# Performance work log

Measured on AMD Instinct MI355X. Metric: run time of the kernel, lower is better.

## Reference

```python
import jax, jax.numpy as jnp
import numpy as np

N_NODES = 50000
N_EDGES = 800000
N_GRAPHS = 512
NEG_SLOPE = 0.2  # PyG GATv2Conv default negative_slope

# layer dims: (in_feat, out_channels, heads)
LAYER_DIMS = [(11, 64, 3), (192, 64, 3), (192, 64, 3), (192, 20, 1)]


def setup_inputs() -> dict:
    key = jax.random.key(0)
    ks = jax.random.split(key, 4 + 6 * len(LAYER_DIMS))
    inp = {}
    inp["x"] = jax.random.normal(ks[0], (N_NODES, 11), jnp.float32)
    src = jax.random.randint(ks[1], (N_EDGES,), 0, N_NODES, dtype=jnp.int32)
    dst = jax.random.randint(ks[2], (N_EDGES,), 0, N_NODES, dtype=jnp.int32)
    inp["edge_index"] = jnp.stack([src, dst])
    inp["batch"] = jnp.sort(jax.random.randint(ks[3], (N_NODES,), 0, N_GRAPHS, dtype=jnp.int32))
    ki = 4
    for li, (fi, ch, h) in enumerate(LAYER_DIMS):
        fo = h * ch
        s = 1.0 / np.sqrt(fi)
        inp[f"Wl{li}"] = jax.random.normal(ks[ki + 0], (fo, fi), jnp.float32) * s
        inp[f"bl{li}"] = jnp.zeros((fo,), jnp.float32)
        inp[f"Wr{li}"] = jax.random.normal(ks[ki + 1], (fo, fi), jnp.float32) * s
        inp[f"br{li}"] = jnp.zeros((fo,), jnp.float32)
        inp[f"att{li}"] = jax.random.normal(ks[ki + 2], (h, ch), jnp.float32) * (1.0 / np.sqrt(ch))
        inp[f"b{li}"] = jnp.zeros((fo,), jnp.float32)
        ki += 6
    return inp


def gatv2_layer(x, src, dst, Wl, bl, Wr, br, att, bias, heads, ch):
    """PyG GATv2Conv (concat=True): e = att . leaky_relu(lin_l(x_j)+lin_r(x_i)),
    alpha = softmax over incoming edges of each dst node, out = sum alpha * lin_l(x_j)."""
    N = x.shape[0]
    xl = (x @ Wl.T + bl).reshape(N, heads, ch)  # source transform [N,H,C]
    xr = (x @ Wr.T + br).reshape(N, heads, ch)  # target transform [N,H,C]
    m = xl[src] + xr[dst]                        # [E,H,C] edge-wise gather
    e = jnp.einsum("ehc,hc->eh", jax.nn.leaky_relu(m, NEG_SLOPE), att)  # [E,H]
    emax = jax.ops.segment_max(e, dst, num_segments=N)   # per-dst softmax (stable)
    p = jnp.exp(e - emax[dst])
    denom = jax.ops.segment_sum(p, dst, num_segments=N)
    alpha = p / denom[dst]                        # [E,H]
    out = jax.ops.segment_sum(xl[src] * alpha[..., None], dst, num_segments=N)
    return out.reshape(N, heads * ch) + bias


def reference(x, edge_index, batch,
              Wl0, bl0, Wr0, br0, att0, b0,
              Wl1, bl1, Wr1, br1, att1, b1,
              Wl2, bl2, Wr2, br2, att2, b2,
              Wl3, bl3, Wr3, br3, att3, b3):
    N = x.shape[0]
    loop = jnp.arange(N, dtype=edge_index.dtype)  # add_self_loops=True
    src = jnp.concatenate([edge_index[0], loop])
    dst = jnp.concatenate([edge_index[1], loop])
    h = gatv2_layer(x, src, dst, Wl0, bl0, Wr0, br0, att0, b0, 3, 64)
    h = jax.nn.relu(h)
    h = gatv2_layer(h, src, dst, Wl1, bl1, Wr1, br1, att1, b1, 3, 64)
    h = jax.nn.relu(h)
    h = gatv2_layer(h, src, dst, Wl2, bl2, Wr2, br2, att2, b2, 3, 64)
    h = jax.nn.relu(h)
    h = gatv2_layer(h, src, dst, Wl3, bl3, Wr3, br3, att3, b3, 1, 20)
    # global_add_pool
    return jax.ops.segment_sum(h, batch, num_segments=N_GRAPHS)  # [G, 20]
```

## Files before the change

### kernel.cpp

```cpp
#include <hip/hip_runtime.h>

#define NN 50000
#define NE 800000
#define NT 850000
#define NG 512
#define NSB 49

typedef __attribute__((ext_vector_type(8))) short bf16x8;
typedef __attribute__((ext_vector_type(4))) float f32x4;


template <int CTRL>
__device__ __forceinline__ float dpp_add(float x) {
  int y = __builtin_amdgcn_update_dpp(0, __float_as_int(x), CTRL, 0xF, 0xF, true);
  return x + __int_as_float(y);
}
template <int CTRL>
__device__ __forceinline__ float dpp_max(float x) {
  int y = __builtin_amdgcn_update_dpp(0, __float_as_int(x), CTRL, 0xF, 0xF, true);
  return fmaxf(x, __int_as_float(y));
}

__device__ __forceinline__ float swz16(float x) {
  return __int_as_float(__builtin_amdgcn_ds_swizzle(__float_as_int(x), 0x401F));
}

__device__ __forceinline__ float rowsum16(float x) {
  x = dpp_add<0xB1>(x);
  x = dpp_add<0x4E>(x);
  x = dpp_add<0x124>(x);
  x = dpp_add<0x128>(x);
  return x;
}
__device__ __forceinline__ float quadsum4(float x) {
  x = dpp_add<0xB1>(x);
  x = dpp_add<0x4E>(x);
  return x;
}
__device__ __forceinline__ float xg_sum(float x) {
  x += swz16(x);
  auto p = __builtin_amdgcn_permlane32_swap(__float_as_uint(x), __float_as_uint(x), false, false);
  return __uint_as_float(p[0]) + __uint_as_float(p[1]);
}
__device__ __forceinline__ float xg_max(float x) {
  x = fmaxf(x, swz16(x));
  auto p = __builtin_amdgcn_permlane32_swap(__float_as_uint(x), __float_as_uint(x), false, false);
  return fmaxf(__uint_as_float(p[0]), __uint_as_float(p[1]));
}
__device__ __forceinline__ float xq_sum(float x) {
  x = dpp_add<0x124>(x);
  x = dpp_add<0x128>(x);
  return xg_sum(x);
}
__device__ __forceinline__ float xq_max(float x) {
  x = dpp_max<0x124>(x);
  x = dpp_max<0x128>(x);
  return xg_max(x);
}

__device__ __forceinline__ float exp2_fast(float x) {
#if __has_builtin(__builtin_amdgcn_exp2f)
  return __builtin_amdgcn_exp2f(x);
#else
  return exp2f(x);
#endif
}

__device__ __forceinline__ float lrelu(float t) { return fmaxf(t, 0.2f * t); }

__device__ __forceinline__ unsigned int f2bf(float f) {
  unsigned int u = __float_as_uint(f);
  u = (u + 0x7FFFu + ((u >> 16) & 1u)) >> 16;
  return u;
}
__device__ __forceinline__ float bf_lo(unsigned int u) { return __uint_as_float(u << 16); }
__device__ __forceinline__ float bf_hi(unsigned int u) { return __uint_as_float(u & 0xFFFF0000u); }
__device__ __forceinline__ float4 bf2f4(uint2 u) {
  return make_float4(bf_lo(u.x), bf_hi(u.x), bf_lo(u.y), bf_hi(u.y));
}

__device__ __forceinline__ void pk_l(float2& d, float2 a, float2 b) {
  asm("v_pk_fma_f32 %0, %1, %2, %0 op_sel_hi:[0,1,1]" : "+v"(d) : "v"(a), "v"(b));
}
__device__ __forceinline__ void pk_h(float2& d, float2 a, float2 b) {
  asm("v_pk_fma_f32 %0, %1, %2, %0 op_sel:[1,0,0]" : "+v"(d) : "v"(a), "v"(b));
}


__global__ void k_hist(const int* __restrict__ dst, int* __restrict__ cnt) {
  int i = blockIdx.x * blockDim.x + threadIdx.x;
  if (i < NT) {
    int d = (i < NE) ? dst[i] : (i - NE);
    atomicAdd(&cnt[d], 1);
  }
}

__global__ __launch_bounds__(1024)
void k_scanA(const int* __restrict__ cnt, int* __restrict__ offs, int* __restrict__ bsum) {
  __shared__ int sh[1024];
  int tid = threadIdx.x;
  int idx = blockIdx.x * 1024 + tid;
  int v = (idx < NN) ? cnt[idx] : 0;
  sh[tid] = v;
  __syncthreads();
  for (int off = 1; off < 1024; off <<= 1) {
    int t = (tid >= off) ? sh[tid - off] : 0;
    __syncthreads();
    sh[tid] += t;
    __syncthreads();
  }
  if (idx < NN) offs[idx] = sh[tid] - v;
  if (tid == 1023) bsum[blockIdx.x] = sh[1023];
}

__global__ void k_scanB(int* __restrict__ bsum, int* __restrict__ offs) {
  int tot = 0;
#pragma unroll 7
  for (int i = 0; i < NSB; ++i) {
    int v = bsum[i];
    bsum[i] = tot;
    tot += v;
  }
  offs[NN] = tot;
}

__global__ __launch_bounds__(1024)
void k_scanC(int* __restrict__ offs, const int* __restrict__ bsum) {
  int idx = blockIdx.x * 1024 + threadIdx.x;
  if (idx < NN) offs[idx] += bsum[blockIdx.x];
}

__global__ void k_scatter(const int* __restrict__ src, const int* __restrict__ dst,
                          const int* __restrict__ offs, int* __restrict__ cur,
                          int* __restrict__ srt) {
  int i = blockIdx.x * blockDim.x + threadIdx.x;
  if (i < NT) {
    int s, d;
    if (i < NE) { s = src[i]; d = dst[i]; }
    else        { s = d = i - NE; }
    int pos = offs[d] + atomicAdd(&cur[d], 1);
    srt[pos] = s;
  }
}

__global__ void k_goffs(const int* __restrict__ batch, int* __restrict__ goffs) {
  int i = blockIdx.x * 256 + threadIdx.x;
  if (i >= NN) return;
  int b = batch[i];
  if (i == 0) {
    for (int g = 0; g <= b; ++g) goffs[g] = 0;
  } else {
    int pb = batch[i - 1];
    for (int g = pb + 1; g <= b; ++g) goffs[g] = i;
  }
  if (i == NN - 1) {
    for (int g = b + 1; g <= NG; ++g) goffs[g] = NN;
  }
}


__global__ void k_cvtW(const float* __restrict__ a, const float* __restrict__ b,
                       const float* __restrict__ c, const float* __restrict__ d,
                       const float* __restrict__ e, const float* __restrict__ f,
                       unsigned short* __restrict__ out) {
  int i = blockIdx.x * 256 + threadIdx.x;
  if (i >= 155136) return;
  float v;
  if      (i < 36864)  v = a[i];
  else if (i < 73728)  v = b[i - 36864];
  else if (i < 110592) v = c[i - 73728];
  else if (i < 147456) v = d[i - 110592];
  else if (i < 151296) v = e[i - 147456];
  else                 v = f[i - 151296];
  out[i] = (unsigned short)f2bf(v);
}


#define LSTR 200

__global__ __launch_bounds__(256)
void k_gemm_mfma2(const unsigned short* __restrict__ Abf,
                  const unsigned short* __restrict__ W1bf,
                  const unsigned short* __restrict__ W2bf,
                  const float* __restrict__ bias1, const float* __restrict__ bias2,
                  unsigned short* __restrict__ C1, unsigned short* __restrict__ C2,
                  int M, int FO) {
  __shared__ unsigned short Al[64 * LSTR];
  __shared__ unsigned short Bl[2][64 * LSTR];
  int tid = threadIdx.x;
  int mb = blockIdx.x * 64;
  int nb = blockIdx.y * 64;

  {
    int r = tid >> 2, q = tid & 3;
    int ga = min(mb + r, M - 1);
    int gb = min(nb + r, FO - 1);
    const unsigned short* pA = Abf  + (size_t)ga * 192 + q * 48;
    const unsigned short* p1 = W1bf + (size_t)gb * 192 + q * 48;
    const unsigned short* p2 = W2bf + (size_t)gb * 192 + q * 48;
    unsigned short* lA = Al + r * LSTR + q * 48;
    unsigned short* l1 = Bl[0] + r * LSTR + q * 48;
    unsigned short* l2 = Bl[1] + r * LSTR + q * 48;
#pragma unroll
    for (int i = 0; i < 6; ++i) {
      *(bf16x8*)(lA + i * 8) = *(const bf16x8*)(pA + i * 8);
      *(bf16x8*)(l1 + i * 8) = *(const bf16x8*)(p1 + i * 8);
      *(bf16x8*)(l2 + i * 8) = *(const bf16x8*)(p2 + i * 8);
    }
  }
  __syncthreads();

  int l = tid & 63, wid = tid >> 6;
  int wr = (wid >> 1) * 32, wc = (wid & 1) * 32;
  int lr = l & 15, lk = (l >> 4) * 8;

  f32x4 acc[2][2][2];
#pragma unroll
  for (int a = 0; a < 2; ++a)
#pragma unroll
    for (int b = 0; b < 2; ++b)
#pragma unroll
      for (int c = 0; c < 2; ++c) acc[a][b][c] = (f32x4){0.f, 0.f, 0.f, 0.f};

  const unsigned short* pa0 = Al + (wr + 0 + lr) * LSTR + lk;
  const unsigned short* pa1 = Al + (wr + 16 + lr) * LSTR + lk;
  const unsigned short* p10 = Bl[0] + (wc + 0 + lr) * LSTR + lk;
  const unsigned short* p11 = Bl[0] + (wc + 16 + lr) * LSTR + lk;
  const unsigned short* p20 = Bl[1] + (wc + 0 + lr) * LSTR + lk;
  const unsigned short* p21 = Bl[1] + (wc + 16 + lr) * LSTR + lk;
#pragma unroll
  for (int kt = 0; kt < 6; ++kt) {
    bf16x8 a0 = *(const bf16x8*)(pa0 + kt * 32);
    bf16x8 a1 = *(const bf16x8*)(pa1 + kt * 32);
    bf16x8 b10 = *(const bf16x8*)(p10 + kt * 32);
    bf16x8 b11 = *(const bf16x8*)(p11 + kt * 32);
    bf16x8 b20 = *(const bf16x8*)(p20 + kt * 32);
    bf16x8 b21 = *(const bf16x8*)(p21 + kt * 32);
    acc[0][0][0] = __builtin_amdgcn_mfma_f32_16x16x32_bf16(a0, b10, acc[0][0][0], 0, 0, 0);
    acc[0][0][1] = __builtin_amdgcn_mfma_f32_16x16x32_bf16(a0, b11, acc[0][0][1], 0, 0, 0);
    acc[0][1][0] = __builtin_amdgcn_mfma_f32_16x16x32_bf16(a1, b10, acc[0][1][0], 0, 0, 0);
    acc[0][1][1] = __builtin_amdgcn_mfma_f32_16x16x32_bf16(a1, b11, acc[0][1][1], 0, 0, 0);
    acc[1][0][0] = __builtin_amdgcn_mfma_f32_16x16x32_bf16(a0, b20, acc[1][0][0], 0, 0, 0);
    acc[1][0][1] = __builtin_amdgcn_mfma_f32_16x16x32_bf16(a0, b21, acc[1][0][1], 0, 0, 0);
    acc[1][1][0] = __builtin_amdgcn_mfma_f32_16x16x32_bf16(a1, b20, acc[1][1][0], 0, 0, 0);
    acc[1][1][1] = __builtin_amdgcn_mfma_f32_16x16x32_bf16(a1, b21, acc[1][1][1], 0, 0, 0);
  }

  int rb = (l >> 4) * 4;
#pragma unroll
  for (int mt = 0; mt < 2; ++mt) {
    unsigned short* C = mt == 0 ? C1 : C2;
    const float* bias = mt == 0 ? bias1 : bias2;
#pragma unroll
    for (int fn = 0; fn < 2; ++fn) {
      int col = nb + wc + fn * 16 + lr;
      if (col >= FO) continue;
      float bv = bias[col];
#pragma unroll
      for (int fm = 0; fm < 2; ++fm) {
        const f32x4& av = acc[mt][fm][fn];
#pragma unroll
        for (int i = 0; i < 4; ++i) {
          int row = mb + wr + fm * 16 + rb + i;
          if (row < M) C[(size_t)row * FO + col] = (unsigned short)f2bf(av[i] + bv);
        }
      }
    }
  }
}


__global__ __launch_bounds__(256)
void k_gemm_dual(const float* __restrict__ A, int M, int K, int FO,
                 const float* __restrict__ W1, const float* __restrict__ bias1,
                 const float* __restrict__ W2, const float* __restrict__ bias2,
                 unsigned short* __restrict__ C1, unsigned short* __restrict__ C2) {
  constexpr int CT = 16;
  constexpr int BN = CT * 4;
  constexpr int BR = (256 / CT) * 8;
  constexpr int AF4 = BR / 64;
  __shared__ float As[16][BR + 4];
  __shared__ float Bs[2][16][BN + 4];

  int tid = threadIdx.x;
  int tx = tid % CT, ty = tid / CT;
  int mb = blockIdx.x * BR, nb = blockIdx.y * BN;
  int nkt = (K + 15) >> 4;

  float4 sa[AF4], sb1, sb2;

  auto ldrow = [&](const float* P, int row, int lim, int k0, int kq) -> float4 {
    float4 v = make_float4(0.f, 0.f, 0.f, 0.f);
    if (row < lim) {
      float t[4];
#pragma unroll
      for (int i = 0; i < 4; ++i)
        t[i] = (k0 + kq + i < K) ? P[(size_t)row * K + k0 + kq + i] : 0.f;
      v = make_float4(t[0], t[1], t[2], t[3]);
    }
    return v;
  };

  auto loadg = [&](int kt) {
    int k0 = kt * 16;
#pragma unroll
    for (int q = 0; q < AF4; ++q) {
      int f4 = q * 256 + tid;
      sa[q] = ldrow(A, mb + (f4 >> 2), M, k0, (f4 & 3) * 4);
    }
    int row = tid >> 2, kq = (tid & 3) * 4;
    sb1 = ldrow(W1, nb + row, FO, k0, kq);
    sb2 = ldrow(W2, nb + row, FO, k0, kq);
  };

  auto stlds = [&]() {
#pragma unroll
    for (int q = 0; q < AF4; ++q) {
      int f4 = q * 256 + tid;
      int row = f4 >> 2, kq = (f4 & 3) * 4;
      As[kq + 0][row] = sa[q].x; As[kq + 1][row] = sa[q].y;
      As[kq + 2][row] = sa[q].z; As[kq + 3][row] = sa[q].w;
    }
    int row = tid >> 2, kq = (tid & 3) * 4;
    Bs[0][kq + 0][row] = sb1.x; Bs[0][kq + 1][row] = sb1.y;
    Bs[0][kq + 2][row] = sb1.z; Bs[0][kq + 3][row] = sb1.w;
    Bs[1][kq + 0][row] = sb2.x; Bs[1][kq + 1][row] = sb2.y;
    Bs[1][kq + 2][row] = sb2.z; Bs[1][kq + 3][row] = sb2.w;
  };

  float2 c1[8][2], c2[8][2];
#pragma unroll
  for (int r = 0; r < 8; ++r)
#pragma unroll
    for (int j = 0; j < 2; ++j) {
      c1[r][j] = make_float2(0.f, 0.f);
      c2[r][j] = make_float2(0.f, 0.f);
    }

  loadg(0);
  stlds();
  __syncthreads();

  for (int t = 0;;) {
#pragma unroll
    for (int k = 0; k < 16; ++k) {
      float4 av0 = *(const float4*)&As[k][ty * 8 + 0];
      float4 av1 = *(const float4*)&As[k][ty * 8 + 4];
      float4 bv1 = *(const float4*)&Bs[0][k][tx * 4];
      float4 bv2 = *(const float4*)&Bs[1][k][tx * 4];
      float2 f1a = make_float2(bv1.x, bv1.y), f1b = make_float2(bv1.z, bv1.w);
      float2 f2a = make_float2(bv2.x, bv2.y), f2b = make_float2(bv2.z, bv2.w);
      float2 a01 = make_float2(av0.x, av0.y), a23 = make_float2(av0.z, av0.w);
      float2 a45 = make_float2(av1.x, av1.y), a67 = make_float2(av1.z, av1.w);
#define PKROW(rp, a)                                                       \
      pk_l(c1[2 * rp + 0][0], a, f1a); pk_l(c1[2 * rp + 0][1], a, f1b);    \
      pk_h(c1[2 * rp + 1][0], a, f1a); pk_h(c1[2 * rp + 1][1], a, f1b);    \
      pk_l(c2[2 * rp + 0][0], a, f2a); pk_l(c2[2 * rp + 0][1], a, f2b);    \
      pk_h(c2[2 * rp + 1][0], a, f2a); pk_h(c2[2 * rp + 1][1], a, f2b);
      PKROW(0, a01) PKROW(1, a23) PKROW(2, a45) PKROW(3, a67)
#undef PKROW
    }
    if (++t == nkt) break;
    loadg(t);
    __syncthreads();
    stlds();
    __syncthreads();
  }

  int col = nb + tx * 4;
  if (col < FO) {
    float4 bb1 = *(const float4*)&bias1[col];
    float4 bb2 = *(const float4*)&bias2[col];
#pragma unroll
    for (int r = 0; r < 8; ++r) {
      int m = mb + ty * 8 + r;
      if (m >= M) continue;
      uint2 o1, o2;
      o1.x = f2bf(c1[r][0].x + bb1.x) | (f2bf(c1[r][0].y + bb1.y) << 16);
      o1.y = f2bf(c1[r][1].x + bb1.z) | (f2bf(c1[r][1].y + bb1.w) << 16);
      o2.x = f2bf(c2[r][0].x + bb2.x) | (f2bf(c2[r][0].y + bb2.y) << 16);
      o2.y = f2bf(c2[r][1].x + bb2.z) | (f2bf(c2[r][1].y + bb2.w) << 16);
      *(uint2*)&C1[(size_t)m * FO + col] = o1;
      *(uint2*)&C2[(size_t)m * FO + col] = o2;
    }
  }
}


__global__ __launch_bounds__(256)
void k_gat3(const unsigned short* __restrict__ xl, const unsigned short* __restrict__ xr,
            const float* __restrict__ att, const float* __restrict__ bias,
            const int* __restrict__ offs, const int* __restrict__ srt,
            unsigned short* __restrict__ obf, int relu) {
  const float L2E = 1.4426950408889634f;
  int lane = threadIdx.x & 63;
  int grp = lane >> 4, lg = lane & 15;
  int n = blockIdx.x * 4 + (threadIdx.x >> 6);
  if (n >= NN) return;

  float4 xrv[3], atv[3];
#pragma unroll
  for (int h = 0; h < 3; ++h) {
    xrv[h] = bf2f4(*(const uint2*)(xr + (size_t)n * 192 + h * 64 + lg * 4));
    float4 a = *(const float4*)&att[h * 64 + lg * 4];
    atv[h] = make_float4(a.x * L2E, a.y * L2E, a.z * L2E, a.w * L2E);
  }
  float m[3] = {-1e30f, -1e30f, -1e30f}, d[3] = {0.f, 0.f, 0.f};
  float4 acc[3];
#pragma unroll
  for (int h = 0; h < 3; ++h) acc[h] = make_float4(0.f, 0.f, 0.f, 0.f);

  int e0 = offs[n], e1 = offs[n + 1];
  int nch = (e1 - e0 + 3) >> 2;

  uint2 Rc[3];
  bool vc;
  int j = e0 + grp;
  {
    int jj = min(j, e1 - 1);
    int s = srt[jj];
    const unsigned short* b = xl + (size_t)s * 192 + lg * 4;
    Rc[0] = *(const uint2*)(b);
    Rc[1] = *(const uint2*)(b + 64);
    Rc[2] = *(const uint2*)(b + 128);
    vc = j < e1;
  }
  for (int it = 0; it < nch; ++it) {
    uint2 Rn[3];
    bool vn = false;
    int jn = j + 4;
    if (it + 1 < nch) {
      int jj = min(jn, e1 - 1);
      int s = srt[jj];
      const unsigned short* b = xl + (size_t)s * 192 + lg * 4;
      Rn[0] = *(const uint2*)(b);
      Rn[1] = *(const uint2*)(b + 64);
      Rn[2] = *(const uint2*)(b + 128);
      vn = jn < e1;
    }
    float4 Xc[3];
    Xc[0] = bf2f4(Rc[0]); Xc[1] = bf2f4(Rc[1]); Xc[2] = bf2f4(Rc[2]);
    float part[3];
#pragma unroll
    for (int h = 0; h < 3; ++h) {
      float t = lrelu(Xc[h].x + xrv[h].x);
      float pa = t * atv[h].x;
      t = lrelu(Xc[h].y + xrv[h].y); pa = fmaf(t, atv[h].y, pa);
      t = lrelu(Xc[h].z + xrv[h].z); pa = fmaf(t, atv[h].z, pa);
      t = lrelu(Xc[h].w + xrv[h].w); pa = fmaf(t, atv[h].w, pa);
      part[h] = pa;
    }
#pragma unroll
    for (int h = 0; h < 3; ++h) {
      part[h] = rowsum16(part[h]);
      part[h] = vc ? part[h] : -1e30f;
    }
    float g = fmaxf(fmaxf(part[0] - m[0], part[1] - m[1]), part[2] - m[2]);
    if (__any(g > 11.0f)) {
#pragma unroll
      for (int h = 0; h < 3; ++h) {
        float nm = fmaxf(m[h], part[h]);
        float sc = exp2_fast(m[h] - nm);
        d[h] *= sc;
        acc[h].x *= sc; acc[h].y *= sc; acc[h].z *= sc; acc[h].w *= sc;
        m[h] = nm;
      }
    }
#pragma unroll
    for (int h = 0; h < 3; ++h) {
      float p = vc ? exp2_fast(part[h] - m[h]) : 0.f;
      d[h] += p;
      acc[h].x = fmaf(p, Xc[h].x, acc[h].x);
      acc[h].y = fmaf(p, Xc[h].y, acc[h].y);
      acc[h].z = fmaf(p, Xc[h].z, acc[h].z);
      acc[h].w = fmaf(p, Xc[h].w, acc[h].w);
    }
    Rc[0] = Rn[0]; Rc[1] = Rn[1]; Rc[2] = Rn[2];
    vc = vn; j = jn;
  }

#pragma unroll
  for (int h = 0; h < 3; ++h) {
    float nm = xg_max(m[h]);
    float sc = exp2_fast(m[h] - nm);
    float D = xg_sum(d[h] * sc);
    float A0 = xg_sum(acc[h].x * sc);
    float A1 = xg_sum(acc[h].y * sc);
    float A2 = xg_sum(acc[h].z * sc);
    float A3 = xg_sum(acc[h].w * sc);
    if (grp == 0) {
      float4 bb = *(const float4*)&bias[h * 64 + lg * 4];
      float inv = 1.0f / D;
      float v0 = fmaf(A0, inv, bb.x);
      float v1 = fmaf(A1, inv, bb.y);
      float v2 = fmaf(A2, inv, bb.z);
      float v3 = fmaf(A3, inv, bb.w);
      if (relu) {
        v0 = fmaxf(v0, 0.f); v1 = fmaxf(v1, 0.f);
        v2 = fmaxf(v2, 0.f); v3 = fmaxf(v3, 0.f);
      }
      unsigned int lo = f2bf(v0) | (f2bf(v1) << 16);
      unsigned int hi = f2bf(v2) | (f2bf(v3) << 16);
      *(uint2*)(obf + (size_t)n * 192 + h * 64 + lg * 4) = make_uint2(lo, hi);
    }
  }
}


__global__ __launch_bounds__(256)
void k_gat1(const unsigned short* __restrict__ xl, const unsigned short* __restrict__ xr,
            const float* __restrict__ att, const float* __restrict__ bias,
            const int* __restrict__ offs, const int* __restrict__ srt,
            float* __restrict__ hout) {
  const float L2E = 1.4426950408889634f;
  int lane = threadIdx.x & 63;
  int grp = lane >> 2, lg = lane & 3;
  int n = blockIdx.x * 4 + (threadIdx.x >> 6);
  if (n >= NN) return;

  float xrv[5], atv[5];
#pragma unroll
  for (int i = 0; i < 5; ++i) {
    xrv[i] = bf_lo(xr[(size_t)n * 20 + lg * 5 + i]);
    atv[i] = att[lg * 5 + i] * L2E;
  }
  float m = -1e30f, d = 0.f, a[5] = {0.f, 0.f, 0.f, 0.f, 0.f};

  int e0 = offs[n], e1 = offs[n + 1];
  int nch = (e1 - e0 + 15) >> 4;

  float Xc[5];
  bool vc;
  int j = e0 + grp;
  {
    int jj = min(j, e1 - 1);
    int s = srt[jj];
    const unsigned short* b = xl + (size_t)s * 20 + lg * 5;
#pragma unroll
    for (int i = 0; i < 5; ++i) Xc[i] = bf_lo(b[i]);
    vc = j < e1;
  }
  for (int it = 0; it < nch; ++it) {
    float Xn[5] = {0.f, 0.f, 0.f, 0.f, 0.f};
    bool vn = false;
    int jn = j + 16;
    if (it + 1 < nch) {
      int jj = min(jn, e1 - 1);
      int s = srt[jj];
      const unsigned short* b = xl + (size_t)s * 20 + lg * 5;
#pragma unroll
      for (int i = 0; i < 5; ++i) Xn[i] = bf_lo(b[i]);
      vn = jn < e1;
    }
    float pa = lrelu(Xc[0] + xrv[0]) * atv[0];
#pragma unroll
    for (int i = 1; i < 5; ++i) pa = fmaf(lrelu(Xc[i] + xrv[i]), atv[i], pa);
    pa = quadsum4(pa);
    pa = vc ? pa : -1e30f;
    if (__any(pa - m > 11.0f)) {
      float nm = fmaxf(m, pa);
      float sc = exp2_fast(m - nm);
      d *= sc;
#pragma unroll
      for (int i = 0; i < 5; ++i) a[i] *= sc;
      m = nm;
    }
    float p = vc ? exp2_fast(pa - m) : 0.f;
    d += p;
#pragma unroll
    for (int i = 0; i < 5; ++i) a[i] = fmaf(p, Xc[i], a[i]);
#pragma unroll
    for (int i = 0; i < 5; ++i) Xc[i] = Xn[i];
    vc = vn; j = jn;
  }

  float nm = xq_max(m);
  float sc = exp2_fast(m - nm);
  float D = xq_sum(d * sc);
  float A[5];
#pragma unroll
  for (int i = 0; i < 5; ++i) A[i] = xq_sum(a[i] * sc);
  if (grp == 0) {
    float inv = 1.0f / D;
    float* o = hout + (size_t)n * 20 + lg * 5;
#pragma unroll
    for (int i = 0; i < 5; ++i)
      o[i] = fmaf(A[i], inv, bias[lg * 5 + i]);
  }
}


__global__ __launch_bounds__(64)
void k_pool(const float* __restrict__ h, const int* __restrict__ goffs,
            float* __restrict__ out) {
  int g = blockIdx.x;
  int lane = threadIdx.x;
  if (lane >= 20) return;
  int s = goffs[g], e = goffs[g + 1];
  float sum = 0.f;
  for (int r = s; r < e; ++r) sum += h[(size_t)r * 20 + lane];
  out[g * 20 + lane] = sum;
}


extern "C" void kernel_launch(void* const* d_in, const int* in_sizes, int n_in,
                              void* d_out, int out_size, void* d_ws, size_t ws_size,
                              hipStream_t stream) {
  const float* x = (const float*)d_in[0];
  const int* src = (const int*)d_in[1];
  const int* dst = src + NE;
  const int* batch = (const int*)d_in[2];
  const float *Wl[4], *bl[4], *Wr[4], *br[4], *att[4], *bb[4];
  for (int li = 0; li < 4; ++li) {
    Wl[li]  = (const float*)d_in[3 + li * 6 + 0];
    bl[li]  = (const float*)d_in[3 + li * 6 + 1];
    Wr[li]  = (const float*)d_in[3 + li * 6 + 2];
    br[li]  = (const float*)d_in[3 + li * 6 + 3];
    att[li] = (const float*)d_in[3 + li * 6 + 4];
    bb[li]  = (const float*)d_in[3 + li * 6 + 5];
  }

  char* p = (char*)d_ws;
  auto alloc = [&](size_t bytes) {
    char* r = p;
    p += (bytes + 255) & ~(size_t)255;
    return r;
  };
  unsigned short* xlbf = (unsigned short*)alloc((size_t)NN * 192 * 2);
  unsigned short* xrbf = (unsigned short*)alloc((size_t)NN * 192 * 2);
  unsigned short* hbf  = (unsigned short*)alloc((size_t)NN * 192 * 2);
  unsigned short* wb   = (unsigned short*)alloc((size_t)155136 * 2);
  int* srt   = (int*)alloc((size_t)NT * 4);
  int* offs  = (int*)alloc((size_t)(NN + 1) * 4);
  int* cnt   = (int*)alloc((size_t)NN * 4);
  int* cur   = (int*)alloc((size_t)NN * 4);
  int* bsum  = (int*)alloc((size_t)NSB * 4);
  int* goffs = (int*)alloc((size_t)(NG + 1) * 4);
  float* hpool = (float*)alloc((size_t)NN * 20 * 4);

  hipMemsetAsync(cnt, 0, (size_t)NN * 4, stream);
  hipMemsetAsync(cur, 0, (size_t)NN * 4, stream);

  k_hist<<<(NT + 255) / 256, 256, 0, stream>>>(dst, cnt);
  k_scanA<<<NSB, 1024, 0, stream>>>(cnt, offs, bsum);
  k_scanB<<<1, 1, 0, stream>>>(bsum, offs);
  k_scanC<<<NSB, 1024, 0, stream>>>(offs, bsum);
  k_scatter<<<(NT + 255) / 256, 256, 0, stream>>>(src, dst, offs, cur, srt);
  k_goffs<<<(NN + 255) / 256, 256, 0, stream>>>(batch, goffs);
  k_cvtW<<<(155136 + 255) / 256, 256, 0, stream>>>(Wl[1], Wr[1], Wl[2], Wr[2], Wl[3], Wr[3], wb);

  {
    dim3 g((NN + 127) / 128, 3);
    k_gemm_dual<<<g, 256, 0, stream>>>(x, NN, 11, 192, Wl[0], bl[0], Wr[0], br[0], xlbf, xrbf);
    k_gat3<<<(NN + 3) / 4, 256, 0, stream>>>(xlbf, xrbf, att[0], bb[0], offs, srt, hbf, 1);
  }
  {
    dim3 gm((NN + 63) / 64, 3);
    k_gemm_mfma2<<<gm, 256, 0, stream>>>(hbf, wb + 0, wb + 36864, bl[1], br[1], xlbf, xrbf, NN, 192);
    k_gat3<<<(NN + 3) / 4, 256, 0, stream>>>(xlbf, xrbf, att[1], bb[1], offs, srt, hbf, 1);
    k_gemm_mfma2<<<gm, 256, 0, stream>>>(hbf, wb + 73728, wb + 110592, bl[2], br[2], xlbf, xrbf, NN, 192);
    k_gat3<<<(NN + 3) / 4, 256, 0, stream>>>(xlbf, xrbf, att[2], bb[2], offs, srt, hbf, 1);
  }
  {
    dim3 gm((NN + 63) / 64, 1);
    k_gemm_mfma2<<<gm, 256, 0, stream>>>(hbf, wb + 147456, wb + 151296, bl[3], br[3], xlbf, xrbf, NN, 20);
    k_gat1<<<(NN + 3) / 4, 256, 0, stream>>>(xlbf, xrbf, att[3], bb[3], offs, srt, hpool);
    k_pool<<<NG, 64, 0, stream>>>(hpool, goffs, (float*)d_out);
  }
}
```

Measured before the change: 523.4 us.

## Drop LDS staging in GEMM, pack GAT math, deepen gather prefetch

The MFMA GEMM kernel now feeds its MFMA operands straight from global memory instead of staging A and both weight tiles in shared memory behind a barrier. The GATv2 aggregation kernel rewrites its per-edge math with packed v_pk_fma_f32 operations on float2 pairs. It also switches from a one-deep to a two-deep software prefetch of neighbour rows, alternating two register buffers. The aims are to remove LDS traffic and the sync, halve VALU instruction count, and hide more gather latency, at the cost of redundant global loads across waves and higher register pressure.

Measured after the change: 583.4 us. +11.5%, slower.

```diff
diff --git a/kernel.cpp b/kernel.cpp
--- a/kernel.cpp
+++ b/kernel.cpp
@@ -75,8 +75,11 @@
 }
 __device__ __forceinline__ float bf_lo(unsigned int u) { return __uint_as_float(u << 16); }
 __device__ __forceinline__ float bf_hi(unsigned int u) { return __uint_as_float(u & 0xFFFF0000u); }
-__device__ __forceinline__ float4 bf2f4(uint2 u) {
-  return make_float4(bf_lo(u.x), bf_hi(u.x), bf_lo(u.y), bf_hi(u.y));
+
+__device__ __forceinline__ float2 pkfma(float2 a, float2 b, float2 c) {
+  float2 d = c;
+  asm("v_pk_fma_f32 %0, %1, %2, %0" : "+v"(d) : "v"(a), "v"(b));
+  return d;
 }
 
 __device__ __forceinline__ void pk_l(float2& d, float2 a, float2 b) {
@@ -176,8 +179,6 @@
 }
 
 
-#define LSTR 200
-
 __global__ __launch_bounds__(256)
 void k_gemm_mfma2(const unsigned short* __restrict__ Abf,
                   const unsigned short* __restrict__ W1bf,
@@ -185,35 +186,23 @@
                   const float* __restrict__ bias1, const float* __restrict__ bias2,
                   unsigned short* __restrict__ C1, unsigned short* __restrict__ C2,
                   int M, int FO) {
-  __shared__ unsigned short Al[64 * LSTR];
-  __shared__ unsigned short Bl[2][64 * LSTR];
   int tid = threadIdx.x;
-  int mb = blockIdx.x * 64;
-  int nb = blockIdx.y * 64;
-
-  {
-    int r = tid >> 2, q = tid & 3;
-    int ga = min(mb + r, M - 1);
-    int gb = min(nb + r, FO - 1);
-    const unsigned short* pA = Abf  + (size_t)ga * 192 + q * 48;
-    const unsigned short* p1 = W1bf + (size_t)gb * 192 + q * 48;
-    const unsigned short* p2 = W2bf + (size_t)gb * 192 + q * 48;
-    unsigned short* lA = Al + r * LSTR + q * 48;
-    unsigned short* l1 = Bl[0] + r * LSTR + q * 48;
-    unsigned short* l2 = Bl[1] + r * LSTR + q * 48;
-#pragma unroll
-    for (int i = 0; i < 6; ++i) {
-      *(bf16x8*)(lA + i * 8) = *(const bf16x8*)(pA + i * 8);
-      *(bf16x8*)(l1 + i * 8) = *(const bf16x8*)(p1 + i * 8);
-      *(bf16x8*)(l2 + i * 8) = *(const bf16x8*)(p2 + i * 8);
-    }
-  }
-  __syncthreads();
-
   int l = tid & 63, wid = tid >> 6;
+  int mb = blockIdx.x * 64, nb = blockIdx.y * 64;
   int wr = (wid >> 1) * 32, wc = (wid & 1) * 32;
   int lr = l & 15, lk = (l >> 4) * 8;
 
+  int ar0 = min(mb + wr +  0 + lr, M - 1);
+  int ar1 = min(mb + wr + 16 + lr, M - 1);
+  int bc0 = min(nb + wc +  0 + lr, FO - 1);
+  int bc1 = min(nb + wc + 16 + lr, FO - 1);
+  const unsigned short* pa0 = Abf  + (size_t)ar0 * 192 + lk;
+  const unsigned short* pa1 = Abf  + (size_t)ar1 * 192 + lk;
+  const unsigned short* q10 = W1bf + (size_t)bc0 * 192 + lk;
+  const unsigned short* q11 = W1bf + (size_t)bc1 * 192 + lk;
+  const unsigned short* q20 = W2bf + (size_t)bc0 * 192 + lk;
+  const unsigned short* q21 = W2bf + (size_t)bc1 * 192 + lk;
+
   f32x4 acc[2][2][2];
 #pragma unroll
   for (int a = 0; a < 2; ++a)
@@ -222,20 +211,14 @@
 #pragma unroll
       for (int c = 0; c < 2; ++c) acc[a][b][c] = (f32x4){0.f, 0.f, 0.f, 0.f};
 
-  const unsigned short* pa0 = Al + (wr + 0 + lr) * LSTR + lk;
-  const unsigned short* pa1 = Al + (wr + 16 + lr) * LSTR + lk;
-  const unsigned short* p10 = Bl[0] + (wc + 0 + lr) * LSTR + lk;
-  const unsigned short* p11 = Bl[0] + (wc + 16 + lr) * LSTR + lk;
-  const unsigned short* p20 = Bl[1] + (wc + 0 + lr) * LSTR + lk;
-  const unsigned short* p21 = Bl[1] + (wc + 16 + lr) * LSTR + lk;
 #pragma unroll
   for (int kt = 0; kt < 6; ++kt) {
-    bf16x8 a0 = *(const bf16x8*)(pa0 + kt * 32);
-    bf16x8 a1 = *(const bf16x8*)(pa1 + kt * 32);
-    bf16x8 b10 = *(const bf16x8*)(p10 + kt * 32);
-    bf16x8 b11 = *(const bf16x8*)(p11 + kt * 32);
-    bf16x8 b20 = *(const bf16x8*)(p20 + kt * 32);
-    bf16x8 b21 = *(const bf16x8*)(p21 + kt * 32);
+    bf16x8 a0  = *(const bf16x8*)(pa0 + kt * 32);
+    bf16x8 a1  = *(const bf16x8*)(pa1 + kt * 32);
+    bf16x8 b10 = *(const bf16x8*)(q10 + kt * 32);
+    bf16x8 b11 = *(const bf16x8*)(q11 + kt * 32);
+    bf16x8 b20 = *(const bf16x8*)(q20 + kt * 32);
+    bf16x8 b21 = *(const bf16x8*)(q21 + kt * 32);
     acc[0][0][0] = __builtin_amdgcn_mfma_f32_16x16x32_bf16(a0, b10, acc[0][0][0], 0, 0, 0);
     acc[0][0][1] = __builtin_amdgcn_mfma_f32_16x16x32_bf16(a0, b11, acc[0][0][1], 0, 0, 0);
     acc[0][1][0] = __builtin_amdgcn_mfma_f32_16x16x32_bf16(a1, b10, acc[0][1][0], 0, 0, 0);
@@ -397,58 +380,56 @@
   int grp = lane >> 4, lg = lane & 15;
   int n = blockIdx.x * 4 + (threadIdx.x >> 6);
   if (n >= NN) return;
-
-  float4 xrv[3], atv[3];
+  const float2 ONE = make_float2(1.f, 1.f);
+  const float2 PT2 = make_float2(0.2f, 0.2f);
+  const float2 ZERO = make_float2(0.f, 0.f);
+
+  float2 xrp[6], atp[6];
 #pragma unroll
   for (int h = 0; h < 3; ++h) {
-    xrv[h] = bf2f4(*(const uint2*)(xr + (size_t)n * 192 + h * 64 + lg * 4));
+    uint2 u = *(const uint2*)(xr + (size_t)n * 192 + h * 64 + lg * 4);
+    xrp[h * 2 + 0] = make_float2(bf_lo(u.x), bf_hi(u.x));
+    xrp[h * 2 + 1] = make_float2(bf_lo(u.y), bf_hi(u.y));
     float4 a = *(const float4*)&att[h * 64 + lg * 4];
-    atv[h] = make_float4(a.x * L2E, a.y * L2E, a.z * L2E, a.w * L2E);
-  }
-  float m[3] = {-1e30f, -1e30f, -1e30f}, d[3] = {0.f, 0.f, 0.f};
-  float4 acc[3];
-#pragma unroll
-  for (int h = 0; h < 3; ++h) acc[h] = make_float4(0.f, 0.f, 0.f, 0.f);
+    atp[h * 2 + 0] = make_float2(a.x * L2E, a.y * L2E);
+    atp[h * 2 + 1] = make_float2(a.z * L2E, a.w * L2E);
+  }
+  float m[3] = {-1e30f, -1e30f, -1e30f}, dd[3] = {0.f, 0.f, 0.f};
+  float2 ac[6] = {ZERO, ZERO, ZERO, ZERO, ZERO, ZERO};
 
   int e0 = offs[n], e1 = offs[n + 1];
   int nch = (e1 - e0 + 3) >> 2;
 
-  uint2 Rc[3];
-  bool vc;
-  int j = e0 + grp;
-  {
+  auto LDQ = [&](int it, uint2* R, bool& v) {
+    int j = e0 + it * 4 + grp;
     int jj = min(j, e1 - 1);
     int s = srt[jj];
     const unsigned short* b = xl + (size_t)s * 192 + lg * 4;
-    Rc[0] = *(const uint2*)(b);
-    Rc[1] = *(const uint2*)(b + 64);
-    Rc[2] = *(const uint2*)(b + 128);
-    vc = j < e1;
-  }
-  for (int it = 0; it < nch; ++it) {
-    uint2 Rn[3];
-    bool vn = false;
-    int jn = j + 4;
-    if (it + 1 < nch) {
-      int jj = min(jn, e1 - 1);
-      int s = srt[jj];
-      const unsigned short* b = xl + (size_t)s * 192 + lg * 4;
-      Rn[0] = *(const uint2*)(b);
-      Rn[1] = *(const uint2*)(b + 64);
-      Rn[2] = *(const uint2*)(b + 128);
-      vn = jn < e1;
-    }
-    float4 Xc[3];
-    Xc[0] = bf2f4(Rc[0]); Xc[1] = bf2f4(Rc[1]); Xc[2] = bf2f4(Rc[2]);
+    R[0] = *(const uint2*)(b);
+    R[1] = *(const uint2*)(b + 64);
+    R[2] = *(const uint2*)(b + 128);
+    v = j < e1;
+  };
+
+  auto BODY = [&](const uint2* R, bool vc) {
+    float2 X[6];
+#pragma unroll
+    for (int h = 0; h < 3; ++h) {
+      X[h * 2 + 0] = make_float2(bf_lo(R[h].x), bf_hi(R[h].x));
+      X[h * 2 + 1] = make_float2(bf_lo(R[h].y), bf_hi(R[h].y));
+    }
     float part[3];
 #pragma unroll
     for (int h = 0; h < 3; ++h) {
-      float t = lrelu(Xc[h].x + xrv[h].x);
-      float pa = t * atv[h].x;
-      t = lrelu(Xc[h].y + xrv[h].y); pa = fmaf(t, atv[h].y, pa);
-      t = lrelu(Xc[h].z + xrv[h].z); pa = fmaf(t, atv[h].z, pa);
-      t = lrelu(Xc[h].w + xrv[h].w); pa = fmaf(t, atv[h].w, pa);
-      part[h] = pa;
+      float2 t0 = pkfma(X[h * 2 + 0], ONE, xrp[h * 2 + 0]);
+      float2 t1 = pkfma(X[h * 2 + 1], ONE, xrp[h * 2 + 1]);
+      float2 u0 = pkfma(t0, PT2, ZERO);
+      float2 u1 = pkfma(t1, PT2, ZERO);
+      float2 l0 = make_float2(fmaxf(t0.x, u0.x), fmaxf(t0.y, u0.y));
+      float2 l1 = make_float2(fmaxf(t1.x, u1.x), fmaxf(t1.y, u1.y));
+      float2 ps = pkfma(l0, atp[h * 2 + 0], ZERO);
+      ps = pkfma(l1, atp[h * 2 + 1], ps);
+      part[h] = ps.x + ps.y;
     }
 #pragma unroll
     for (int h = 0; h < 3; ++h) {
@@ -461,33 +442,55 @@
       for (int h = 0; h < 3; ++h) {
         float nm = fmaxf(m[h], part[h]);
         float sc = exp2_fast(m[h] - nm);
-        d[h] *= sc;
-        acc[h].x *= sc; acc[h].y *= sc; acc[h].z *= sc; acc[h].w *= sc;
+        dd[h] *= sc;
+        float2 SC = make_float2(sc, sc);
+        ac[h * 2 + 0] = pkfma(ac[h * 2 + 0], SC, ZERO);
+        ac[h * 2 + 1] = pkfma(ac[h * 2 + 1], SC, ZERO);
         m[h] = nm;
       }
     }
 #pragma unroll
     for (int h = 0; h < 3; ++h) {
       float p = vc ? exp2_fast(part[h] - m[h]) : 0.f;
-      d[h] += p;
-      acc[h].x = fmaf(p, Xc[h].x, acc[h].x);
-      acc[h].y = fmaf(p, Xc[h].y, acc[h].y);
-      acc[h].z = fmaf(p, Xc[h].z, acc[h].z);
-      acc[h].w = fmaf(p, Xc[h].w, acc[h].w);
-    }
-    Rc[0] = Rn[0]; Rc[1] = Rn[1]; Rc[2] = Rn[2];
-    vc = vn; j = jn;
+      dd[h] += p;
+      float2 P = make_float2(p, p);
+      ac[h * 2 + 0] = pkfma(X[h * 2 + 0], P, ac[h * 2 + 0]);
+      ac[h * 2 + 1] = pkfma(X[h * 2 + 1], P, ac[h * 2 + 1]);
+    }
+  };
+
+  uint2 RA[3], RB[3];
+  bool vA = false, vB = false;
+  if (nch > 0) LDQ(0, RA, vA);
+  if (nch > 1) LDQ(1, RB, vB);
+
+  int it = 0;
+  while (it < nch) {
+    {
+      uint2 T[3]; bool vT = false;
+      if (it + 2 < nch) LDQ(it + 2, T, vT);
+      BODY(RA, vA);
+      RA[0] = T[0]; RA[1] = T[1]; RA[2] = T[2]; vA = vT;
+    }
+    if (++it >= nch) break;
+    {
+      uint2 T[3]; bool vT = false;
+      if (it + 2 < nch) LDQ(it + 2, T, vT);
+      BODY(RB, vB);
+      RB[0] = T[0]; RB[1] = T[1]; RB[2] = T[2]; vB = vT;
+    }
+    ++it;
   }
 
 #pragma unroll
   for (int h = 0; h < 3; ++h) {
     float nm = xg_max(m[h]);
     float sc = exp2_fast(m[h] - nm);
-    float D = xg_sum(d[h] * sc);
-    float A0 = xg_sum(acc[h].x * sc);
-    float A1 = xg_sum(acc[h].y * sc);
-    float A2 = xg_sum(acc[h].z * sc);
-    float A3 = xg_sum(acc[h].w * sc);
+    float D  = xg_sum(dd[h] * sc);
+    float A0 = xg_sum(ac[h * 2 + 0].x * sc);
+    float A1 = xg_sum(ac[h * 2 + 0].y * sc);
+    float A2 = xg_sum(ac[h * 2 + 1].x * sc);
+    float A3 = xg_sum(ac[h * 2 + 1].y * sc);
     if (grp == 0) {
       float4 bb = *(const float4*)&bias[h * 64 + lg * 4];
       float inv = 1.0f / D;
```
